# Kernel optimization log

Hardware: AMD Instinct MI355X
Metric: run time of the kernel (lower is better)

## Reference

```python
import jax, jax.numpy as jnp
import numpy as np

N = 4096          # total nodes
G = 8             # graphs in batch
M_PER = N // G    # nodes per graph (contiguous batch ids)
DEG = 8           # random out-edges per node before symmetrization (~16 after)


def setup_inputs() -> dict:
    rng = np.random.default_rng(0)
    A = np.zeros((N, N), dtype=np.float32)
    for g in range(G):
        lo = g * M_PER
        u = rng.integers(lo, lo + M_PER, size=M_PER * DEG)
        v = rng.integers(lo, lo + M_PER, size=M_PER * DEG)
        A[u, v] = 1.0
        ring = np.arange(lo, lo + M_PER)           # guarantee no isolated nodes
        A[ring, np.roll(ring, -1)] = 1.0
    A = np.maximum(A, A.T)                          # undirected (symmetric)
    np.fill_diagonal(A, 0.0)                        # no self loops
    batch = np.repeat(np.arange(G), M_PER).astype(np.int64)
    return {"A": jnp.asarray(A), "batch": jnp.asarray(batch), "num_graphs": G}


def _netsimile_node_features(A):
    # Vectorized form of the per-node ego-network loop.
    # Row n of M1 is the boolean mask of the 1-hop egonet {n} U N(n);
    # B = M1 @ A counts, for each (n, v), edges from ego1(n) into v, so
    # M2 = M1 | (B > 0) is the 2-hop egonet mask. All loop statistics become
    # row reductions of these matrices.
    n = A.shape[0]
    deg = A.sum(axis=1)                                  # [N] feat0: degree
    deg_safe = jnp.maximum(deg, 1.0)
    f0 = deg
    f2 = jnp.where(deg > 0, (A @ deg) / deg_safe, 0.0)   # scatter_mean(deg[col], row)

    eye = jnp.eye(n, dtype=A.dtype)
    M1 = jnp.maximum(A, eye)                             # [N,N] 1-hop ego masks
    B = M1 @ A                                           # [N,N] one-step reach counts
    f4_raw = (B * M1).sum(axis=1)                        # directed edges inside ego1
    M2 = jnp.maximum(M1, (B > 0).astype(A.dtype))        # [N,N] 2-hop ego masks
    f5 = M2 @ deg - 2.0 * f4_raw                         # sum(mask2[row]) - 2*feat4 (incl. post-loop -=)
    f6 = M2.sum(axis=1) - deg - 1.0                      # |ego2| - deg - 1

    denom = jnp.where(deg > 1, deg * (deg - 1.0), 1.0)
    f1 = jnp.where(deg > 1, (f4_raw - deg) / denom, 0.0)  # clustering coeff
    # undirected graph corrections (data.is_undirected() is True)
    f1 = f1 * 2.0
    f4 = f4_raw / 2.0
    f3 = jnp.where(deg > 0, (A @ f1) / deg_safe, 0.0)     # scatter_mean(f1[col], row)
    return jnp.stack([f0, f1, f2, f3, f4, f5, f6], axis=1)  # [N,7]


def reference(A, batch, num_graphs):
    feat = _netsimile_node_features(A)                   # [N,7]
    n, F = feat.shape
    m = n // num_graphs                                  # equal-size contiguous graphs
    xg = feat.reshape(num_graphs, m, F)                  # batch ids are sorted blocks
    mean = xg.mean(axis=1)                               # [G,7]
    c = xg - mean[:, None, :]
    m2 = (c ** 2).mean(axis=1)
    m3 = (c ** 3).mean(axis=1)
    m4 = (c ** 4).mean(axis=1)
    # torch.median returns the LOWER middle element for even counts
    median = jnp.sort(xg, axis=1)[:, (m - 1) // 2, :]
    eps = jnp.float32(1e-4)
    skew = m3 / jnp.maximum(m2 ** 1.5, eps)
    kurt = m4 / jnp.maximum(m2 ** 2, eps)
    return jnp.hstack([mean, median, jnp.sqrt(m2), skew, kurt])  # [G,35]
```

## Files before the change

kernel.cpp:

```cpp
#include <hip/hip_runtime.h>
#include <stdint.h>

typedef unsigned long long u64;

#define NNODE 4096
#define NG    8
#define M     512
#define W     8

#define OFF_MASK 0
#define OFF_DEG  (262144)
#define OFF_F1   (262144 + 16384)
#define OFF_FEAT (262144 + 32768)

__global__ __launch_bounds__(256) void k_pack(const float* __restrict__ A,
                                              u64* __restrict__ gmask,
                                              float* __restrict__ gdeg) {
    int row  = (blockIdx.x << 2) + (threadIdx.x >> 6);
    int lane = threadIdx.x & 63;
    int lo   = (row >> 9) << 9;
    const float* rowp = A + (size_t)row * NNODE + lo;
    float4 a = *(const float4*)(rowp + lane * 8);
    float4 b = *(const float4*)(rowp + lane * 8 + 4);
    unsigned int byte =
        (a.x != 0.f ? 1u : 0u) | (a.y != 0.f ? 2u : 0u) |
        (a.z != 0.f ? 4u : 0u) | (a.w != 0.f ? 8u : 0u) |
        (b.x != 0.f ? 16u : 0u) | (b.y != 0.f ? 32u : 0u) |
        (b.z != 0.f ? 64u : 0u) | (b.w != 0.f ? 128u : 0u);
    ((unsigned char*)gmask)[(size_t)row * 64 + lane] = (unsigned char)byte;
    int c = __popc(byte);
#pragma unroll
    for (int off = 32; off; off >>= 1) c += __shfl_down(c, off, 64);
    if (lane == 0) gdeg[row] = (float)c;
}

__global__ __launch_bounds__(256) void k_feat(const u64* __restrict__ gmask,
                                              const float* __restrict__ gdeg,
                                              float* __restrict__ featg,
                                              float* __restrict__ f1g) {
    int g = blockIdx.x >> 1, half = blockIdx.x & 1;
    int t = threadIdx.x;
    __shared__ u64 smT[W * M];
    __shared__ float sdeg[M];
    __shared__ u64 planes[9][W];

    const u64* gm = gmask + (size_t)g * M * W;
    for (int idx = t; idx < M * W; idx += 256) {
        int u = idx >> 3, w = idx & 7;
        smT[w * M + u] = gm[idx];
    }
    for (int i = t; i < M; i += 256) sdeg[i] = gdeg[g * M + i];
    __syncthreads();

    int wv = t >> 6, lane = t & 63;
    for (int w = wv; w < W; w += 4) {
        int d = (int)sdeg[(w << 6) + lane];
#pragma unroll
        for (int k = 0; k < 9; k++) {
            u64 bal = __ballot(((d >> k) & 1) != 0);
            if (lane == 0) planes[k][w] = bal;
        }
    }
    __syncthreads();

    int n = half * 256 + t;
    u64 arow[W], m1[W], reach[W];
#pragma unroll
    for (int w = 0; w < W; w++) {
        arow[w] = smT[w * M + n];
        m1[w] = arow[w];
        reach[w] = 0ull;
    }
    m1[n >> 6] |= 1ull << (n & 63);

    int f4 = 0;
    for (int w = 0; w < W; w++) {
        u64 bits = m1[w];
        while (bits) {
            int b = __ffsll(bits) - 1;
            bits &= bits - 1;
            int u = (w << 6) + b;
#pragma unroll
            for (int w2 = 0; w2 < W; w2++) {
                u64 r = smT[w2 * M + u];
                reach[w2] |= r;
                f4 += __popcll(r & m1[w2]);
            }
        }
    }
    int f6c = 0;
    u64 m2m[W];
#pragma unroll
    for (int w = 0; w < W; w++) { m2m[w] = m1[w] | reach[w]; f6c += __popcll(m2m[w]); }
    int f5i = 0, f2i = 0;
#pragma unroll
    for (int k = 0; k < 9; k++) {
        int c5 = 0, c2 = 0;
#pragma unroll
        for (int w = 0; w < W; w++) {
            c5 += __popcll(m2m[w] & planes[k][w]);
            c2 += __popcll(arow[w] & planes[k][w]);
        }
        f5i += c5 << k;
        f2i += c2 << k;
    }
    float deg = sdeg[n];
    float f4raw = (float)f4;
    float f1 = (deg > 1.f) ? 2.f * (f4raw - deg) / (deg * (deg - 1.f)) : 0.f;
    float* fb = featg + (size_t)g * 7 * M;
    fb[0 * M + n] = deg;
    fb[1 * M + n] = f1;
    fb[2 * M + n] = (deg > 0.f) ? (float)f2i / deg : 0.f;
    fb[4 * M + n] = f4raw * 0.5f;
    fb[5 * M + n] = (float)f5i - 2.f * f4raw;
    fb[6 * M + n] = (float)f6c - deg - 1.f;
    f1g[g * M + n] = f1;
}

__global__ __launch_bounds__(512) void k_f3(const u64* __restrict__ gmask,
                                            const float* __restrict__ gdeg,
                                            const float* __restrict__ f1g,
                                            float* __restrict__ featg) {
    int g = blockIdx.x;
    int t = threadIdx.x;
    __shared__ float f1s[M];
    f1s[t] = f1g[g * M + t];
    __syncthreads();

    const u64* m = gmask + ((size_t)g * M + t) * W;
    float sum = 0.f;
#pragma unroll
    for (int w = 0; w < W; w++) {
        u64 bits = m[w];
        while (bits) {
            int b = __ffsll(bits) - 1;
            bits &= bits - 1;
            sum += f1s[(w << 6) + b];
        }
    }
    float deg = gdeg[g * M + t];
    featg[(size_t)g * 7 * M + 3 * M + t] = (deg > 0.f) ? sum / deg : 0.f;
}

__global__ __launch_bounds__(256) void k_stats(const float* __restrict__ featg,
                                               float* __restrict__ out) {
    int blk = blockIdx.x;
    int gf = blk >> 1, half = blk & 1;
    int g = gf / 7, f = gf % 7;
    int t = threadIdx.x;
    __shared__ __align__(16) float sv[M];
    __shared__ double rsum[4], r2[4], r3[4], r4[4];
    __shared__ double smean;

    sv[t]       = featg[(size_t)gf * M + t];
    sv[t + 256] = featg[(size_t)gf * M + t + 256];
    __syncthreads();

    int wv = t >> 6, lane = t & 63;
    if (half == 0) {
        double s = (double)sv[t] + (double)sv[t + 256];
#pragma unroll
        for (int off = 32; off; off >>= 1) s += __shfl_xor(s, off, 64);
        if (lane == 0) rsum[wv] = s;
        __syncthreads();
        if (t == 0) smean = (rsum[0] + rsum[1] + rsum[2] + rsum[3]) * (1.0 / 512.0);
        __syncthreads();
        double mean = smean;
        double c1 = (double)sv[t] - mean, c2v = (double)sv[t + 256] - mean;
        double a2 = c1 * c1, b2 = c2v * c2v;
        double p2 = a2 + b2, p3 = a2 * c1 + b2 * c2v, p4 = a2 * a2 + b2 * b2;
#pragma unroll
        for (int off = 32; off; off >>= 1) {
            p2 += __shfl_xor(p2, off, 64);
            p3 += __shfl_xor(p3, off, 64);
            p4 += __shfl_xor(p4, off, 64);
        }
        if (lane == 0) { r2[wv] = p2; r3[wv] = p3; r4[wv] = p4; }
        __syncthreads();
        if (t == 0) {
            double m2 = (r2[0] + r2[1] + r2[2] + r2[3]) * (1.0 / 512.0);
            double m3 = (r3[0] + r3[1] + r3[2] + r3[3]) * (1.0 / 512.0);
            double m4 = (r4[0] + r4[1] + r4[2] + r4[3]) * (1.0 / 512.0);
            double sd = sqrt(m2);
            double den3 = m2 * sd;  if (den3 < 1e-4) den3 = 1e-4;
            double den4 = m2 * m2;  if (den4 < 1e-4) den4 = 1e-4;
            out[g * 35 + f]      = (float)smean;
            out[g * 35 + 14 + f] = (float)sd;
            out[g * 35 + 21 + f] = (float)(m3 / den3);
            out[g * 35 + 28 + f] = (float)(m4 / den4);
        }
    }

    float cv = sv[half * 256 + t];
    int less = 0, eq = 0;
    for (int j = 0; j < M; j += 4) {
        float4 x = *(const float4*)&sv[j];
        less += (x.x < cv) + (x.y < cv) + (x.z < cv) + (x.w < cv);
        eq   += (x.x == cv) + (x.y == cv) + (x.z == cv) + (x.w == cv);
    }
    if (less <= 255 && less + eq > 255) out[g * 35 + 7 + f] = cv;
}

extern "C" void kernel_launch(void* const* d_in, const int* in_sizes, int n_in,
                              void* d_out, int out_size, void* d_ws, size_t ws_size,
                              hipStream_t stream) {
    const float* A = (const float*)d_in[0];
    float* out = (float*)d_out;
    char* ws = (char*)d_ws;
    u64*   gmask = (u64*)(ws + OFF_MASK);
    float* gdeg  = (float*)(ws + OFF_DEG);
    float* f1g   = (float*)(ws + OFF_F1);
    float* featg = (float*)(ws + OFF_FEAT);

    k_pack <<<NNODE / 4, 256, 0, stream>>>(A, gmask, gdeg);
    k_feat <<<NG * 2,    256, 0, stream>>>(gmask, gdeg, featg, f1g);
    k_f3   <<<NG,        512, 0, stream>>>(gmask, gdeg, f1g, featg);
    k_stats<<<NG * 7 * 2, 256, 0, stream>>>(featg, out);
}
```

Measured before the change: 120.0 us.

## Fuse pack, feature, f3 and stats kernels into one per-graph block

Replaces four kernel launches with a single kernel of one 1024-thread block per graph. The block packs its diagonal adjacency block straight into shared-memory bitmasks, computes degrees, features, f3 and the statistics entirely in shared memory. This removes three launch gaps and the global workspace round-trips. In exchange only 8 blocks run, so the pack phase reads 8 MB of A with very little parallelism, and the feature phase uses 512 threads per block instead of 16 blocks.

```diff
diff --git a/kernel.cpp b/kernel.cpp
--- a/kernel.cpp
+++ b/kernel.cpp
@@ -8,197 +8,171 @@
 #define M     512
 #define W     8
 
-#define OFF_MASK 0
-#define OFF_DEG  (262144)
-#define OFF_F1   (262144 + 16384)
-#define OFF_FEAT (262144 + 32768)
+__global__ __launch_bounds__(1024) void k_all(const float* __restrict__ A,
+                                              float* __restrict__ out) {
+    int g    = blockIdx.x;
+    int t    = threadIdx.x;
+    int wv   = t >> 6, lane = t & 63;
 
-__global__ __launch_bounds__(256) void k_pack(const float* __restrict__ A,
-                                              u64* __restrict__ gmask,
-                                              float* __restrict__ gdeg) {
-    int row  = (blockIdx.x << 2) + (threadIdx.x >> 6);
-    int lane = threadIdx.x & 63;
-    int lo   = (row >> 9) << 9;
-    const float* rowp = A + (size_t)row * NNODE + lo;
-    float4 a = *(const float4*)(rowp + lane * 8);
-    float4 b = *(const float4*)(rowp + lane * 8 + 4);
-    unsigned int byte =
-        (a.x != 0.f ? 1u : 0u) | (a.y != 0.f ? 2u : 0u) |
-        (a.z != 0.f ? 4u : 0u) | (a.w != 0.f ? 8u : 0u) |
-        (b.x != 0.f ? 16u : 0u) | (b.y != 0.f ? 32u : 0u) |
-        (b.z != 0.f ? 64u : 0u) | (b.w != 0.f ? 128u : 0u);
-    ((unsigned char*)gmask)[(size_t)row * 64 + lane] = (unsigned char)byte;
-    int c = __popc(byte);
-#pragma unroll
-    for (int off = 32; off; off >>= 1) c += __shfl_down(c, off, 64);
-    if (lane == 0) gdeg[row] = (float)c;
-}
+    __shared__ __align__(16) u64 smT[W * M];
+    __shared__ int   sdegi[M];
+    __shared__ u64   planes[9][W];
+    __shared__ float f1s[M];
+    __shared__ __align__(16) float sfeat[7][M];
+    __shared__ double rsum[7][2];
+    __shared__ double smean[7];
 
-__global__ __launch_bounds__(256) void k_feat(const u64* __restrict__ gmask,
-                                              const float* __restrict__ gdeg,
-                                              float* __restrict__ featg,
-                                              float* __restrict__ f1g) {
-    int g = blockIdx.x >> 1, half = blockIdx.x & 1;
-    int t = threadIdx.x;
-    __shared__ u64 smT[W * M];
-    __shared__ float sdeg[M];
-    __shared__ u64 planes[9][W];
-
-    const u64* gm = gmask + (size_t)g * M * W;
-    for (int idx = t; idx < M * W; idx += 256) {
-        int u = idx >> 3, w = idx & 7;
-        smT[w * M + u] = gm[idx];
+    const float* Ab = A + ((size_t)(g * M)) * NNODE + g * M;
+#pragma unroll 8
+    for (int k = 0; k < 32; k++) {
+        int r = wv * 32 + k;
+        const float* rowp = Ab + (size_t)r * NNODE;
+        float4 a = *(const float4*)(rowp + lane * 8);
+        float4 b = *(const float4*)(rowp + lane * 8 + 4);
+        unsigned int byte =
+            (a.x != 0.f ? 1u : 0u) | (a.y != 0.f ? 2u : 0u) |
+            (a.z != 0.f ? 4u : 0u) | (a.w != 0.f ? 8u : 0u) |
+            (b.x != 0.f ? 16u : 0u) | (b.y != 0.f ? 32u : 0u) |
+            (b.z != 0.f ? 64u : 0u) | (b.w != 0.f ? 128u : 0u);
+        ((unsigned char*)smT)[((size_t)(lane >> 3) * M + r) * 8 + (lane & 7)] =
+            (unsigned char)byte;
     }
-    for (int i = t; i < M; i += 256) sdeg[i] = gdeg[g * M + i];
     __syncthreads();
 
-    int wv = t >> 6, lane = t & 63;
-    for (int w = wv; w < W; w += 4) {
-        int d = (int)sdeg[(w << 6) + lane];
+    u64 arow[W];
+    int degi = 0;
+    if (t < M) {
+#pragma unroll
+        for (int w = 0; w < W; w++) {
+            arow[w] = smT[w * M + t];
+            degi += __popcll(arow[w]);
+        }
+        sdegi[t] = degi;
+    }
+    __syncthreads();
+    if (wv < W) {
+        int d = sdegi[(wv << 6) + lane];
 #pragma unroll
         for (int k = 0; k < 9; k++) {
             u64 bal = __ballot(((d >> k) & 1) != 0);
-            if (lane == 0) planes[k][w] = bal;
+            if (lane == 0) planes[k][wv] = bal;
         }
     }
     __syncthreads();
 
-    int n = half * 256 + t;
-    u64 arow[W], m1[W], reach[W];
+    if (t < M) {
+        u64 m1[W], reach[W];
 #pragma unroll
-    for (int w = 0; w < W; w++) {
-        arow[w] = smT[w * M + n];
-        m1[w] = arow[w];
-        reach[w] = 0ull;
-    }
-    m1[n >> 6] |= 1ull << (n & 63);
+        for (int w = 0; w < W; w++) { m1[w] = arow[w]; reach[w] = 0ull; }
+        m1[t >> 6] |= 1ull << (t & 63);
 
-    int f4 = 0;
-    for (int w = 0; w < W; w++) {
-        u64 bits = m1[w];
-        while (bits) {
-            int b = __ffsll(bits) - 1;
-            bits &= bits - 1;
-            int u = (w << 6) + b;
+        int f4 = 0;
+        for (int w = 0; w < W; w++) {
+            u64 bits = m1[w];
+            while (bits) {
+                int b = __ffsll(bits) - 1;
+                bits &= bits - 1;
+                int u = (w << 6) + b;
 #pragma unroll
-            for (int w2 = 0; w2 < W; w2++) {
-                u64 r = smT[w2 * M + u];
-                reach[w2] |= r;
-                f4 += __popcll(r & m1[w2]);
+                for (int w2 = 0; w2 < W; w2++) {
+                    u64 r = smT[w2 * M + u];
+                    reach[w2] |= r;
+                    f4 += __popcll(r & m1[w2]);
+                }
             }
         }
+        int f6c = 0;
+        u64 m2m[W];
+#pragma unroll
+        for (int w = 0; w < W; w++) { m2m[w] = m1[w] | reach[w]; f6c += __popcll(m2m[w]); }
+        int f5i = 0, f2i = 0;
+#pragma unroll
+        for (int k = 0; k < 9; k++) {
+            int c5 = 0, c2 = 0;
+#pragma unroll
+            for (int w = 0; w < W; w++) {
+                c5 += __popcll(m2m[w] & planes[k][w]);
+                c2 += __popcll(arow[w] & planes[k][w]);
+            }
+            f5i += c5 << k;
+            f2i += c2 << k;
+        }
+        float deg = (float)degi;
+        float f4raw = (float)f4;
+        float f1 = (deg > 1.f) ? 2.f * (f4raw - deg) / (deg * (deg - 1.f)) : 0.f;
+        sfeat[0][t] = deg;
+        sfeat[1][t] = f1;
+        sfeat[2][t] = (deg > 0.f) ? (float)f2i / deg : 0.f;
+        sfeat[4][t] = f4raw * 0.5f;
+        sfeat[5][t] = (float)f5i - 2.f * f4raw;
+        sfeat[6][t] = (float)f6c - deg - 1.f;
+        f1s[t] = f1;
     }
-    int f6c = 0;
-    u64 m2m[W];
-#pragma unroll
-    for (int w = 0; w < W; w++) { m2m[w] = m1[w] | reach[w]; f6c += __popcll(m2m[w]); }
-    int f5i = 0, f2i = 0;
-#pragma unroll
-    for (int k = 0; k < 9; k++) {
-        int c5 = 0, c2 = 0;
+    __syncthreads();
+
+    if (t < M) {
+        float sum = 0.f;
 #pragma unroll
         for (int w = 0; w < W; w++) {
-            c5 += __popcll(m2m[w] & planes[k][w]);
-            c2 += __popcll(arow[w] & planes[k][w]);
+            u64 bits = arow[w];
+            while (bits) {
+                int b = __ffsll(bits) - 1;
+                bits &= bits - 1;
+                sum += f1s[(w << 6) + b];
+            }
         }
-        f5i += c5 << k;
-        f2i += c2 << k;
+        sfeat[3][t] = (degi > 0) ? sum / (float)degi : 0.f;
     }
-    float deg = sdeg[n];
-    float f4raw = (float)f4;
-    float f1 = (deg > 1.f) ? 2.f * (f4raw - deg) / (deg * (deg - 1.f)) : 0.f;
-    float* fb = featg + (size_t)g * 7 * M;
-    fb[0 * M + n] = deg;
-    fb[1 * M + n] = f1;
-    fb[2 * M + n] = (deg > 0.f) ? (float)f2i / deg : 0.f;
-    fb[4 * M + n] = f4raw * 0.5f;
-    fb[5 * M + n] = (float)f5i - 2.f * f4raw;
-    fb[6 * M + n] = (float)f6c - deg - 1.f;
-    f1g[g * M + n] = f1;
-}
-
-__global__ __launch_bounds__(512) void k_f3(const u64* __restrict__ gmask,
-                                            const float* __restrict__ gdeg,
-                                            const float* __restrict__ f1g,
-                                            float* __restrict__ featg) {
-    int g = blockIdx.x;
-    int t = threadIdx.x;
-    __shared__ float f1s[M];
-    f1s[t] = f1g[g * M + t];
     __syncthreads();
 
-    const u64* m = gmask + ((size_t)g * M + t) * W;
-    float sum = 0.f;
+    if (wv < 7) {
+        int f = wv;
+        float vals[8];
+        double s = 0.0;
 #pragma unroll
-    for (int w = 0; w < W; w++) {
-        u64 bits = m[w];
-        while (bits) {
-            int b = __ffsll(bits) - 1;
-            bits &= bits - 1;
-            sum += f1s[(w << 6) + b];
-        }
-    }
-    float deg = gdeg[g * M + t];
-    featg[(size_t)g * 7 * M + 3 * M + t] = (deg > 0.f) ? sum / deg : 0.f;
-}
-
-__global__ __launch_bounds__(256) void k_stats(const float* __restrict__ featg,
-                                               float* __restrict__ out) {
-    int blk = blockIdx.x;
-    int gf = blk >> 1, half = blk & 1;
-    int g = gf / 7, f = gf % 7;
-    int t = threadIdx.x;
-    __shared__ __align__(16) float sv[M];
-    __shared__ double rsum[4], r2[4], r3[4], r4[4];
-    __shared__ double smean;
-
-    sv[t]       = featg[(size_t)gf * M + t];
-    sv[t + 256] = featg[(size_t)gf * M + t + 256];
-    __syncthreads();
-
-    int wv = t >> 6, lane = t & 63;
-    if (half == 0) {
-        double s = (double)sv[t] + (double)sv[t + 256];
+        for (int k = 0; k < 8; k++) { vals[k] = sfeat[f][lane + 64 * k]; s += (double)vals[k]; }
 #pragma unroll
         for (int off = 32; off; off >>= 1) s += __shfl_xor(s, off, 64);
-        if (lane == 0) rsum[wv] = s;
-        __syncthreads();
-        if (t == 0) smean = (rsum[0] + rsum[1] + rsum[2] + rsum[3]) * (1.0 / 512.0);
-        __syncthreads();
-        double mean = smean;
-        double c1 = (double)sv[t] - mean, c2v = (double)sv[t + 256] - mean;
-        double a2 = c1 * c1, b2 = c2v * c2v;
-        double p2 = a2 + b2, p3 = a2 * c1 + b2 * c2v, p4 = a2 * a2 + b2 * b2;
+        double mean = s * (1.0 / 512.0);
+        double c2 = 0.0, c3 = 0.0, c4 = 0.0;
+#pragma unroll
+        for (int k = 0; k < 8; k++) {
+            double c = (double)vals[k] - mean;
+            double cc = c * c;
+            c2 += cc; c3 += cc * c; c4 += cc * cc;
+        }
 #pragma unroll
         for (int off = 32; off; off >>= 1) {
-            p2 += __shfl_xor(p2, off, 64);
-            p3 += __shfl_xor(p3, off, 64);
-            p4 += __shfl_xor(p4, off, 64);
+            c2 += __shfl_xor(c2, off, 64);
+            c3 += __shfl_xor(c3, off, 64);
+            c4 += __shfl_xor(c4, off, 64);
         }
-        if (lane == 0) { r2[wv] = p2; r3[wv] = p3; r4[wv] = p4; }
-        __syncthreads();
-        if (t == 0) {
-            double m2 = (r2[0] + r2[1] + r2[2] + r2[3]) * (1.0 / 512.0);
-            double m3 = (r3[0] + r3[1] + r3[2] + r3[3]) * (1.0 / 512.0);
-            double m4 = (r4[0] + r4[1] + r4[2] + r4[3]) * (1.0 / 512.0);
+        if (lane == 0) {
+            double m2 = c2 * (1.0 / 512.0);
+            double m3 = c3 * (1.0 / 512.0);
+            double m4 = c4 * (1.0 / 512.0);
             double sd = sqrt(m2);
             double den3 = m2 * sd;  if (den3 < 1e-4) den3 = 1e-4;
             double den4 = m2 * m2;  if (den4 < 1e-4) den4 = 1e-4;
-            out[g * 35 + f]      = (float)smean;
+            out[g * 35 + f]      = (float)mean;
             out[g * 35 + 14 + f] = (float)sd;
             out[g * 35 + 21 + f] = (float)(m3 / den3);
             out[g * 35 + 28 + f] = (float)(m4 / den4);
         }
+        (void)rsum; (void)smean;
     }
 
-    float cv = sv[half * 256 + t];
-    int less = 0, eq = 0;
-    for (int j = 0; j < M; j += 4) {
-        float4 x = *(const float4*)&sv[j];
-        less += (x.x < cv) + (x.y < cv) + (x.z < cv) + (x.w < cv);
-        eq   += (x.x == cv) + (x.y == cv) + (x.z == cv) + (x.w == cv);
+    for (int T = t; T < 7 * M; T += 1024) {
+        int f = T >> 9, i = T & (M - 1);
+        float cv = sfeat[f][i];
+        int less = 0, eq = 0;
+        for (int j = 0; j < M; j += 4) {
+            float4 x = *(const float4*)&sfeat[f][j];
+            less += (x.x < cv) + (x.y < cv) + (x.z < cv) + (x.w < cv);
+            eq   += (x.x == cv) + (x.y == cv) + (x.z == cv) + (x.w == cv);
+        }
+        if (less <= 255 && less + eq > 255) out[g * 35 + 7 + f] = cv;
     }
-    if (less <= 255 && less + eq > 255) out[g * 35 + 7 + f] = cv;
 }
 
 extern "C" void kernel_launch(void* const* d_in, const int* in_sizes, int n_in,
@@ -206,14 +180,5 @@
                               hipStream_t stream) {
     const float* A = (const float*)d_in[0];
     float* out = (float*)d_out;
-    char* ws = (char*)d_ws;
-    u64*   gmask = (u64*)(ws + OFF_MASK);
-    float* gdeg  = (float*)(ws + OFF_DEG);
-    float* f1g   = (float*)(ws + OFF_F1);
-    float* featg = (float*)(ws + OFF_FEAT);
-
-    k_pack <<<NNODE / 4, 256, 0, stream>>>(A, gmask, gdeg);
-    k_feat <<<NG * 2,    256, 0, stream>>>(gmask, gdeg, featg, f1g);
-    k_f3   <<<NG,        512, 0, stream>>>(gmask, gdeg, f1g, featg);
-    k_stats<<<NG * 7 * 2, 256, 0, stream>>>(featg, out);
+    k_all<<<NG, 1024, 0, stream>>>(A, out);
 }
```

After: 190.0 us. 1.58x slower.

## Split each node's egonet traversal across four lanes with shuffle reduction

Applied to the files above, without the earlier changes.

The feature kernel now assigns four threads per node, each walking two of the eight 64-bit mask words of the 1-hop egonet, and combines f4 counts and reach bitmasks with xor shuffles. The grid grows from 16 to 64 blocks, so more of the GPU's compute units take part in the dominant 2-hop traversal. In exchange, each block still reloads the full graph mask into shared memory (four times more total loads), and only one lane in four does the final feature write. The adjacency row is rebuilt from m1 by clearing the self bit.

```diff
diff --git a/kernel.cpp b/kernel.cpp
--- a/kernel.cpp
+++ b/kernel.cpp
@@ -34,11 +34,16 @@
     if (lane == 0) gdeg[row] = (float)c;
 }
 
+static __device__ __forceinline__ u64 shfl_xor_u64(u64 v, int mask) {
+    return ((u64)(unsigned)__shfl_xor((int)(v >> 32), mask, 64) << 32) |
+           (u64)(unsigned)__shfl_xor((int)(v & 0xffffffffu), mask, 64);
+}
+
 __global__ __launch_bounds__(256) void k_feat(const u64* __restrict__ gmask,
                                               const float* __restrict__ gdeg,
                                               float* __restrict__ featg,
                                               float* __restrict__ f1g) {
-    int g = blockIdx.x >> 1, half = blockIdx.x & 1;
+    int g = blockIdx.x >> 3, chunk = blockIdx.x & 7;
     int t = threadIdx.x;
     __shared__ u64 smT[W * M];
     __shared__ float sdeg[M];
@@ -63,18 +68,17 @@
     }
     __syncthreads();
 
-    int n = half * 256 + t;
-    u64 arow[W], m1[W], reach[W];
-#pragma unroll
-    for (int w = 0; w < W; w++) {
-        arow[w] = smT[w * M + n];
-        m1[w] = arow[w];
-        reach[w] = 0ull;
-    }
+    int nl = t >> 2, q = t & 3;
+    int n  = chunk * 64 + nl;
+    u64 m1[W], reach[W];
+#pragma unroll
+    for (int w = 0; w < W; w++) { m1[w] = smT[w * M + n]; reach[w] = 0ull; }
     m1[n >> 6] |= 1ull << (n & 63);
 
     int f4 = 0;
-    for (int w = 0; w < W; w++) {
+#pragma unroll
+    for (int wq = 0; wq < 2; wq++) {
+        int w = 2 * q + wq;
         u64 bits = m1[w];
         while (bits) {
             int b = __ffsll(bits) - 1;
@@ -88,33 +92,45 @@
             }
         }
     }
-    int f6c = 0;
-    u64 m2m[W];
-#pragma unroll
-    for (int w = 0; w < W; w++) { m2m[w] = m1[w] | reach[w]; f6c += __popcll(m2m[w]); }
-    int f5i = 0, f2i = 0;
-#pragma unroll
-    for (int k = 0; k < 9; k++) {
-        int c5 = 0, c2 = 0;
-#pragma unroll
-        for (int w = 0; w < W; w++) {
-            c5 += __popcll(m2m[w] & planes[k][w]);
-            c2 += __popcll(arow[w] & planes[k][w]);
-        }
-        f5i += c5 << k;
-        f2i += c2 << k;
-    }
-    float deg = sdeg[n];
-    float f4raw = (float)f4;
-    float f1 = (deg > 1.f) ? 2.f * (f4raw - deg) / (deg * (deg - 1.f)) : 0.f;
-    float* fb = featg + (size_t)g * 7 * M;
-    fb[0 * M + n] = deg;
-    fb[1 * M + n] = f1;
-    fb[2 * M + n] = (deg > 0.f) ? (float)f2i / deg : 0.f;
-    fb[4 * M + n] = f4raw * 0.5f;
-    fb[5 * M + n] = (float)f5i - 2.f * f4raw;
-    fb[6 * M + n] = (float)f6c - deg - 1.f;
-    f1g[g * M + n] = f1;
+    f4 += __shfl_xor(f4, 1, 64);
+    f4 += __shfl_xor(f4, 2, 64);
+#pragma unroll
+    for (int w = 0; w < W; w++) {
+        reach[w] |= shfl_xor_u64(reach[w], 1);
+        reach[w] |= shfl_xor_u64(reach[w], 2);
+    }
+
+    if (q == 0) {
+        int f6c = 0;
+        u64 m2m[W];
+#pragma unroll
+        for (int w = 0; w < W; w++) { m2m[w] = m1[w] | reach[w]; f6c += __popcll(m2m[w]); }
+        int f5i = 0, f2i = 0;
+        u64 arow_self = 1ull << (n & 63);
+#pragma unroll
+        for (int k = 0; k < 9; k++) {
+            int c5 = 0, c2 = 0;
+#pragma unroll
+            for (int w = 0; w < W; w++) {
+                u64 ar = (w == (n >> 6)) ? (m1[w] & ~arow_self) : m1[w];
+                c5 += __popcll(m2m[w] & planes[k][w]);
+                c2 += __popcll(ar & planes[k][w]);
+            }
+            f5i += c5 << k;
+            f2i += c2 << k;
+        }
+        float deg = sdeg[n];
+        float f4raw = (float)f4;
+        float f1 = (deg > 1.f) ? 2.f * (f4raw - deg) / (deg * (deg - 1.f)) : 0.f;
+        float* fb = featg + (size_t)g * 7 * M;
+        fb[0 * M + n] = deg;
+        fb[1 * M + n] = f1;
+        fb[2 * M + n] = (deg > 0.f) ? (float)f2i / deg : 0.f;
+        fb[4 * M + n] = f4raw * 0.5f;
+        fb[5 * M + n] = (float)f5i - 2.f * f4raw;
+        fb[6 * M + n] = (float)f6c - deg - 1.f;
+        f1g[g * M + n] = f1;
+    }
 }
 
 __global__ __launch_bounds__(512) void k_f3(const u64* __restrict__ gmask,
@@ -213,7 +229,7 @@
     float* featg = (float*)(ws + OFF_FEAT);
 
     k_pack <<<NNODE / 4, 256, 0, stream>>>(A, gmask, gdeg);
-    k_feat <<<NG * 2,    256, 0, stream>>>(gmask, gdeg, featg, f1g);
+    k_feat <<<NG * 8,    256, 0, stream>>>(gmask, gdeg, featg, f1g);
     k_f3   <<<NG,        512, 0, stream>>>(gmask, gdeg, f1g, featg);
     k_stats<<<NG * 7 * 2, 256, 0, stream>>>(featg, out);
 }
```

After: 114.2 us. 1.05x faster.
